# Performance work log

Measured on AMD Instinct MI355X. Metric: run time of the kernel, lower is better.

## Reference

```python
import jax, jax.numpy as jnp
import numpy as np

HEADS = 8
DIM_HEAD = 64
SCALE = DIM_HEAD ** (-0.5)


def setup_inputs() -> dict:
    key = jax.random.key(0)
    k1, k2, k3, k4 = jax.random.split(key, 4)
    B, H, W, n, dim = 2, 64, 64, 8, 512
    inner = HEADS * DIM_HEAD  # 512
    x = jax.random.normal(k1, (B, H, W, n, dim), dtype=jnp.float32)
    mask = jax.random.uniform(k2, (B, H, W, 1, n, n), dtype=jnp.float32)
    w_qkv = jax.random.normal(k3, (dim, 3 * inner), dtype=jnp.float32) * 0.02
    w_out = jax.random.normal(k4, (inner, dim), dtype=jnp.float32) * 0.02
    b_out = jnp.zeros((dim,), dtype=jnp.float32)
    return {"x": x, "mask": mask, "w_qkv": w_qkv, "w_out": w_out, "b_out": b_out}


def reference(x, mask, w_qkv, w_out, b_out):
    B, H, W, n, dim = x.shape
    inner = HEADS * DIM_HEAD
    qkv = x @ w_qkv  # [B,H,W,n,3*inner]
    q, k, v = jnp.split(qkv, 3, axis=-1)

    def to_heads(t):
        # 'B H W n (h d) -> B H W h n d'
        t = t.reshape(B, H, W, n, HEADS, DIM_HEAD)
        return jnp.swapaxes(t, 3, 4)

    q, k, v = to_heads(q), to_heads(k), to_heads(v)
    dots = jnp.einsum('bxyhnd,bxyhmd->bxyhnm', q, k) * SCALE
    dots = dots * mask  # multiplicative mask pre-softmax
    attn = jax.nn.softmax(dots, axis=-1)
    out = jnp.einsum('bxyhnm,bxyhmd->bxyhnd', attn, v)
    # 'B H W h n d -> B H W n (h d)'
    out = jnp.swapaxes(out, 3, 4).reshape(B, H, W, n, inner)
    return out @ w_out + b_out
```

## Files before the change

### kernel.cpp

```cpp
#include <hip/hip_runtime.h>
#include <hip/hip_bf16.h>

#define NROWS 65536
#define DIM   512
#define SCALE_ 0.125f

typedef short bf16x8 __attribute__((ext_vector_type(8)));
typedef unsigned short u16x8 __attribute__((ext_vector_type(8)));
typedef float f32x4 __attribute__((ext_vector_type(4)));

__device__ __forceinline__ unsigned short f2bf(float f) {
  union { float f; unsigned u; } v; v.f = f;
  unsigned r = v.u + 0x7FFFu + ((v.u >> 16) & 1u);
  return (unsigned short)(r >> 16);
}

#define GLL16(gptr, lptr) \
  __builtin_amdgcn_global_load_lds((const __attribute__((address_space(1))) void*)(gptr), \
                                   (__attribute__((address_space(3))) void*)(lptr), 16, 0, 0)

__global__ void prep_w_kernel(const float* __restrict__ wqkv,
                              const float* __restrict__ wout,
                              unsigned short* __restrict__ wqkvT,
                              unsigned short* __restrict__ woutT) {
  int idx = blockIdx.x * 256 + threadIdx.x;
  if (idx < 1536 * 512) {
    int j = idx >> 9, c = idx & 511;
    wqkvT[idx] = f2bf(wqkv[(size_t)c * 1536 + j]);
  } else {
    int k2 = idx - 1536 * 512;
    int n = k2 >> 9, c = k2 & 511;
    woutT[k2] = f2bf(wout[(size_t)c * 512 + n]);
  }
}

__global__ void prep_x_kernel(const float* __restrict__ x,
                              unsigned short* __restrict__ xb) {
  size_t i = ((size_t)blockIdx.x * 256 + threadIdx.x) * 8;
  float4 a = *(const float4*)(x + i);
  float4 b = *(const float4*)(x + i + 4);
  u16x8 p;
  p[0] = f2bf(a.x); p[1] = f2bf(a.y); p[2] = f2bf(a.z); p[3] = f2bf(a.w);
  p[4] = f2bf(b.x); p[5] = f2bf(b.y); p[6] = f2bf(b.z); p[7] = f2bf(b.w);
  *(u16x8*)(xb + i) = p;
}

template<int AMODE>
__global__ __launch_bounds__(256, 2)
void qkv_attn_kernel(const float* __restrict__ x,
                     const unsigned short* __restrict__ xb,
                     const float* __restrict__ mask,
                     const unsigned short* __restrict__ wqkvT,
                     unsigned short* __restrict__ attn_out) {
  __shared__ __align__(16) unsigned char smem[81920];

  const int t = threadIdx.x;
  const int lane = t & 63, wave = t >> 6;
  const int wm = wave >> 1, wn = wave & 1;
  const int fr = lane & 15, fq = lane >> 4;
  const int l8 = lane >> 3;
  const int cswz = ((lane & 7) ^ l8) * 8;

  const int per = gridDim.x >> 3;
  const int lin = (blockIdx.x & 7) * per + (blockIdx.x >> 3);
  const int mtile = lin >> 3, head = lin & 7;
  const int r0 = mtile * 128;

  f32x4 acc[4][6];
  const f32x4 z4 = {0.f, 0.f, 0.f, 0.f};
  #pragma unroll
  for (int m = 0; m < 4; ++m)
    #pragma unroll
    for (int n = 0; n < 6; ++n) acc[m][n] = z4;

  auto STAGE = [&](int buf, int kt2) {
    unsigned char* base = smem + buf * 40960;
    const int k0 = kt2 * 64;
    if constexpr (AMODE == 0) {
      const unsigned short* gA = xb + (size_t)(r0 + l8) * 512 + k0 + cswz;
      #pragma unroll
      for (int i = 0; i < 4; ++i) {
        int c = wave * 4 + i;
        GLL16(gA + (size_t)c * 8 * 512, base + c * 1024);
      }
    } else {
      #pragma unroll
      for (int i2 = 0; i2 < 8; ++i2) {
        int c = t + (i2 << 8);
        int row = c >> 4, q = c & 15;
        float4 v = *(const float4*)(x + (size_t)(r0 + row) * 512 + k0 + q * 4);
        ushort4 p;
        p.x = f2bf(v.x); p.y = f2bf(v.y); p.z = f2bf(v.z); p.w = f2bf(v.w);
        unsigned byte = (unsigned)row * 128 +
                        ((((unsigned)(q >> 1)) << 4) ^ (((unsigned)(row & 7)) << 4)) +
                        (unsigned)(q & 1) * 8;
        *(ushort4*)(base + byte) = p;
      }
    }
    const unsigned short* gB = wqkvT + k0 + cswz;
    #pragma unroll
    for (int i = 0; i < 6; ++i) {
      int c = wave * 6 + i;
      int n = c * 8 + l8;
      int jg = ((n >> 6) << 9) + head * 64 + (n & 63);
      GLL16(gB + (size_t)jg * 512, base + 16384 + c * 1024);
    }
  };

  STAGE(0, 0);
  asm volatile("s_waitcnt vmcnt(0)" ::: "memory");
  __syncthreads();
  int cur = 0;

  for (int kt = 0; kt < 8; ++kt) {
    if (kt < 7) STAGE(cur ^ 1, kt + 1);
    unsigned char* Ab = smem + cur * 40960;
    unsigned char* Bb = Ab + 16384;
    const unsigned xr = ((unsigned)(fr & 7)) << 4;
    #pragma unroll
    for (int kk = 0; kk < 2; ++kk) {
      const unsigned ko = ((unsigned)(kk * 64 + fq * 16)) ^ xr;
      bf16x8 a[4], b[6];
      #pragma unroll
      for (int m = 0; m < 4; ++m)
        a[m] = *(const bf16x8*)(Ab + (unsigned)(wm * 64 + m * 16 + fr) * 128 + ko);
      #pragma unroll
      for (int n = 0; n < 6; ++n)
        b[n] = *(const bf16x8*)(Bb + (unsigned)(wn * 96 + n * 16 + fr) * 128 + ko);
      #pragma unroll
      for (int m = 0; m < 4; ++m)
        #pragma unroll
        for (int n = 0; n < 6; ++n)
          acc[m][n] = __builtin_amdgcn_mfma_f32_16x16x32_bf16(a[m], b[n], acc[m][n], 0, 0, 0);
    }
    asm volatile("s_waitcnt vmcnt(0)" ::: "memory");
    __syncthreads();
    cur ^= 1;
  }

  unsigned short* Qs = (unsigned short*)smem;
  unsigned short* Ks = (unsigned short*)(smem + 16384);
  unsigned short* VT = (unsigned short*)(smem + 32768);
  unsigned short* Pl = (unsigned short*)(smem + 52224);

  {
    int d = t >> 2, q = t & 3;
    ushort4 z; z.x = 0; z.y = 0; z.z = 0; z.w = 0;
    *(ushort4*)(VT + d * 152 + 128 + q * 4) = z;
  }
  #pragma unroll
  for (int n = 0; n < 6; ++n) {
    int col = wn * 96 + n * 16 + fr;
    #pragma unroll
    for (int m = 0; m < 4; ++m) {
      if (col < 128) {
        unsigned short* T = (col < 64) ? Qs : Ks;
        unsigned cc = (unsigned)(col & 63);
        #pragma unroll
        for (int r = 0; r < 4; ++r) {
          int row = wm * 64 + m * 16 + fq * 4 + r;
          unsigned byte = (unsigned)row * 128 + ((cc * 2) ^ (((unsigned)(row & 7)) << 4));
          *(unsigned short*)((unsigned char*)T + byte) = f2bf(acc[m][n][r]);
        }
      } else {
        int d = col - 128;
        ushort4 p;
        p.x = f2bf(acc[m][n][0]); p.y = f2bf(acc[m][n][1]);
        p.z = f2bf(acc[m][n][2]); p.w = f2bf(acc[m][n][3]);
        *(ushort4*)(VT + d * 152 + (wm * 64 + m * 16 + fq * 4)) = p;
      }
    }
  }
  __syncthreads();

  #pragma unroll
  for (int pp = 0; pp < 2; ++pp) {
    const int pair = wave * 2 + pp;
    const unsigned rbyte = (unsigned)(pair * 16 + fr) * 128;
    const unsigned xrp = ((unsigned)(fr & 7)) << 4;
    f32x4 s = {0.f, 0.f, 0.f, 0.f};
    #pragma unroll
    for (int kk = 0; kk < 2; ++kk) {
      const unsigned ko = ((unsigned)(kk * 64 + fq * 16)) ^ xrp;
      bf16x8 qf = *(const bf16x8*)((unsigned char*)Qs + rbyte + ko);
      bf16x8 kf = *(const bf16x8*)((unsigned char*)Ks + rbyte + ko);
      s = __builtin_amdgcn_mfma_f32_16x16x32_bf16(qf, kf, s, 0, 0, 0);
    }
    float p4[4];
    #pragma unroll
    for (int r = 0; r < 4; ++r) {
      int row = fq * 4 + r;
      bool valid = (row >> 3) == (fr >> 3);
      int Pg = mtile * 16 + pair * 2 + (row >> 3);
      float mv = mask[(size_t)Pg * 64 + (row & 7) * 8 + (fr & 7)];
      p4[r] = valid ? s[r] * SCALE_ * mv : -3.0e38f;
    }
    #pragma unroll
    for (int r = 0; r < 4; ++r) {
      float v = p4[r];
      float mx = v;
      mx = fmaxf(mx, __shfl_xor(mx, 1));
      mx = fmaxf(mx, __shfl_xor(mx, 2));
      mx = fmaxf(mx, __shfl_xor(mx, 4));
      float e = __expf(v - mx);
      float sm = e;
      sm += __shfl_xor(sm, 1);
      sm += __shfl_xor(sm, 2);
      sm += __shfl_xor(sm, 4);
      p4[r] = e / sm;
    }
    #pragma unroll
    for (int r = 0; r < 4; ++r) {
      int row = fq * 4 + r;
      bool valid = (row >> 3) == (fr >> 3);
      Pl[pair * 640 + row * 40 + fr] = valid ? f2bf(p4[r]) : (unsigned short)0;
      Pl[pair * 640 + row * 40 + 16 + fr] = 0;
    }
    #pragma unroll
    for (int dblk = 0; dblk < 4; ++dblk) {
      bf16x8 af = *(const bf16x8*)((unsigned char*)VT +
                    (unsigned)(dblk * 16 + fr) * 304 + (unsigned)(pair * 32 + fq * 16));
      bf16x8 bf = *(const bf16x8*)((unsigned char*)Pl +
                    (unsigned)pair * 1280 + (unsigned)fr * 80 + (unsigned)fq * 16);
      f32x4 o = {0.f, 0.f, 0.f, 0.f};
      o = __builtin_amdgcn_mfma_f32_16x16x32_bf16(af, bf, o, 0, 0, 0);
      ushort4 pk;
      pk.x = f2bf(o[0]); pk.y = f2bf(o[1]); pk.z = f2bf(o[2]); pk.w = f2bf(o[3]);
      *(ushort4*)(attn_out + (size_t)(r0 + pair * 16 + fr) * 512 +
                  head * 64 + dblk * 16 + fq * 4) = pk;
    }
  }
}

__global__ __launch_bounds__(256, 2)
void outproj_kernel(const unsigned short* __restrict__ attn,
                    const unsigned short* __restrict__ woutT,
                    const float* __restrict__ bias,
                    float* __restrict__ out) {
  __shared__ __align__(16) unsigned short A2[128 * 72];
  __shared__ __align__(16) unsigned short B2[128 * 72];
  const int t = threadIdx.x;
  const int lane = t & 63, wave = t >> 6;
  const int wm = wave >> 1, wn = wave & 1;
  const int fr = lane & 15, fq = lane >> 4;

  const int per = gridDim.x >> 3;
  const int lin = (blockIdx.x & 7) * per + (blockIdx.x >> 3);
  const int mtile = lin >> 2, nt = lin & 3;
  const int r0 = mtile * 128, n0 = nt * 128;

  f32x4 acc[4][4];
  const f32x4 z4 = {0.f, 0.f, 0.f, 0.f};
  #pragma unroll
  for (int m = 0; m < 4; ++m)
    #pragma unroll
    for (int n = 0; n < 4; ++n) acc[m][n] = z4;

  for (int kt = 0; kt < 8; ++kt) {
    const int k0 = kt * 64;
    #pragma unroll
    for (int i2 = 0; i2 < 4; ++i2) {
      int c = t + (i2 << 8);
      int row = c >> 3, wi = c & 7;
      *(uint4*)(A2 + row * 72 + wi * 8) =
          *(const uint4*)(attn + (size_t)(r0 + row) * 512 + k0 + wi * 8);
      *(uint4*)(B2 + row * 72 + wi * 8) =
          *(const uint4*)(woutT + (size_t)(n0 + row) * 512 + k0 + wi * 8);
    }
    __syncthreads();
    #pragma unroll
    for (int kk = 0; kk < 2; ++kk) {
      const int krd = kk * 32 + fq * 8;
      bf16x8 a[4], b[4];
      #pragma unroll
      for (int m = 0; m < 4; ++m)
        a[m] = *(const bf16x8*)(A2 + (wm * 64 + m * 16 + fr) * 72 + krd);
      #pragma unroll
      for (int n = 0; n < 4; ++n)
        b[n] = *(const bf16x8*)(B2 + (wn * 64 + n * 16 + fr) * 72 + krd);
      #pragma unroll
      for (int m = 0; m < 4; ++m)
        #pragma unroll
        for (int n = 0; n < 4; ++n)
          acc[m][n] = __builtin_amdgcn_mfma_f32_16x16x32_bf16(a[m], b[n], acc[m][n], 0, 0, 0);
    }
    __syncthreads();
  }
  #pragma unroll
  for (int n = 0; n < 4; ++n) {
    int col = n0 + wn * 64 + n * 16 + fr;
    float bv = bias[col];
    #pragma unroll
    for (int m = 0; m < 4; ++m) {
      #pragma unroll
      for (int j = 0; j < 4; ++j) {
        int row = r0 + wm * 64 + m * 16 + fq * 4 + j;
        out[(size_t)row * 512 + col] = acc[m][n][j] + bv;
      }
    }
  }
}

extern "C" void kernel_launch(void* const* d_in, const int* in_sizes, int n_in,
                              void* d_out, int out_size, void* d_ws, size_t ws_size,
                              hipStream_t stream) {
  const float* x    = (const float*)d_in[0];
  const float* mask = (const float*)d_in[1];
  const float* wqkv = (const float*)d_in[2];
  const float* wout = (const float*)d_in[3];
  const float* bias = (const float*)d_in[4];
  float* out = (float*)d_out;

  unsigned char* ws = (unsigned char*)d_ws;
  unsigned short* attn  = (unsigned short*)ws;
  unsigned short* wqkvT = (unsigned short*)(ws + 67108864);
  unsigned short* woutT = (unsigned short*)(ws + 67108864 + 1572864);
  unsigned short* xb    = (unsigned short*)(ws + 67108864 + 1572864 + 524288);
  const size_t need_xb = 67108864ull + 1572864ull + 524288ull + 67108864ull;

  prep_w_kernel<<<4096, 256, 0, stream>>>(wqkv, wout, wqkvT, woutT);
  if (ws_size >= need_xb) {
    prep_x_kernel<<<16384, 256, 0, stream>>>(x, xb);
    qkv_attn_kernel<0><<<4096, 256, 0, stream>>>(x, xb, mask, wqkvT, attn);
  } else {
    qkv_attn_kernel<1><<<4096, 256, 0, stream>>>(x, xb, mask, wqkvT, attn);
  }
  outproj_kernel<<<2048, 256, 0, stream>>>(attn, woutT, bias, out);
}
```

Baseline: 238.9 us.

## Fuse x bf16 conversion into QKV kernel with register prefetch; double-buffer out-proj

Removes the separate fp32-to-bf16 pass over x. The QKV kernel now loads fp32 x tiles into registers one step ahead, converts them and writes them to LDS after the MFMA block, so the global loads overlap compute. The mask values are preloaded into registers at kernel start, and the output projection moves to double-buffered global_load_lds staging with a swizzled LDS layout. This saves a full read and write of the x tensor, at the cost of more registers in the QKV kernel and 8x more fp32 reads per tile than the bf16 path, since x is re-read by each of the 8 heads.

```diff
diff --git a/kernel.cpp b/kernel.cpp
--- a/kernel.cpp
+++ b/kernel.cpp
@@ -34,21 +34,8 @@
   }
 }
 
-__global__ void prep_x_kernel(const float* __restrict__ x,
-                              unsigned short* __restrict__ xb) {
-  size_t i = ((size_t)blockIdx.x * 256 + threadIdx.x) * 8;
-  float4 a = *(const float4*)(x + i);
-  float4 b = *(const float4*)(x + i + 4);
-  u16x8 p;
-  p[0] = f2bf(a.x); p[1] = f2bf(a.y); p[2] = f2bf(a.z); p[3] = f2bf(a.w);
-  p[4] = f2bf(b.x); p[5] = f2bf(b.y); p[6] = f2bf(b.z); p[7] = f2bf(b.w);
-  *(u16x8*)(xb + i) = p;
-}
-
-template<int AMODE>
 __global__ __launch_bounds__(256, 2)
 void qkv_attn_kernel(const float* __restrict__ x,
-                     const unsigned short* __restrict__ xb,
                      const float* __restrict__ mask,
                      const unsigned short* __restrict__ wqkvT,
                      unsigned short* __restrict__ attn_out) {
@@ -66,6 +53,18 @@
   const int mtile = lin >> 3, head = lin & 7;
   const int r0 = mtile * 128;
 
+  float mreg[2][4];
+  #pragma unroll
+  for (int pp = 0; pp < 2; ++pp) {
+    int pair = wave * 2 + pp;
+    #pragma unroll
+    for (int r = 0; r < 4; ++r) {
+      int row = fq * 4 + r;
+      int Pg = mtile * 16 + pair * 2 + (row >> 3);
+      mreg[pp][r] = mask[(size_t)Pg * 64 + (row & 7) * 8 + (fr & 7)];
+    }
+  }
+
   f32x4 acc[4][6];
   const f32x4 z4 = {0.f, 0.f, 0.f, 0.f};
   #pragma unroll
@@ -73,47 +72,50 @@
     #pragma unroll
     for (int n = 0; n < 6; ++n) acc[m][n] = z4;
 
-  auto STAGE = [&](int buf, int kt2) {
+  float4 va[8];
+  const int arow = t >> 4, aq = t & 15;
+  const unsigned abyte = (unsigned)arow * 128 +
+                         ((((unsigned)(aq >> 1)) << 4) ^ (((unsigned)(arow & 7)) << 4)) +
+                         (unsigned)(aq & 1) * 8;
+
+  auto LOAD_A = [&](int kt2) {
+    const int k0 = kt2 * 64;
+    const float* gx = x + (size_t)(r0 + arow) * 512 + k0 + aq * 4;
+    #pragma unroll
+    for (int i2 = 0; i2 < 8; ++i2)
+      va[i2] = *(const float4*)(gx + (size_t)i2 * 16 * 512);
+  };
+  auto WRITE_A = [&](int buf) {
     unsigned char* base = smem + buf * 40960;
-    const int k0 = kt2 * 64;
-    if constexpr (AMODE == 0) {
-      const unsigned short* gA = xb + (size_t)(r0 + l8) * 512 + k0 + cswz;
-      #pragma unroll
-      for (int i = 0; i < 4; ++i) {
-        int c = wave * 4 + i;
-        GLL16(gA + (size_t)c * 8 * 512, base + c * 1024);
-      }
-    } else {
-      #pragma unroll
-      for (int i2 = 0; i2 < 8; ++i2) {
-        int c = t + (i2 << 8);
-        int row = c >> 4, q = c & 15;
-        float4 v = *(const float4*)(x + (size_t)(r0 + row) * 512 + k0 + q * 4);
-        ushort4 p;
-        p.x = f2bf(v.x); p.y = f2bf(v.y); p.z = f2bf(v.z); p.w = f2bf(v.w);
-        unsigned byte = (unsigned)row * 128 +
-                        ((((unsigned)(q >> 1)) << 4) ^ (((unsigned)(row & 7)) << 4)) +
-                        (unsigned)(q & 1) * 8;
-        *(ushort4*)(base + byte) = p;
-      }
-    }
-    const unsigned short* gB = wqkvT + k0 + cswz;
+    #pragma unroll
+    for (int i2 = 0; i2 < 8; ++i2) {
+      ushort4 p;
+      p.x = f2bf(va[i2].x); p.y = f2bf(va[i2].y);
+      p.z = f2bf(va[i2].z); p.w = f2bf(va[i2].w);
+      *(ushort4*)(base + abyte + (unsigned)i2 * 2048) = p;
+    }
+  };
+  auto STAGE_B = [&](int buf, int kt2) {
+    unsigned char* base = smem + buf * 40960 + 16384;
+    const unsigned short* gB = wqkvT + kt2 * 64 + cswz;
     #pragma unroll
     for (int i = 0; i < 6; ++i) {
       int c = wave * 6 + i;
       int n = c * 8 + l8;
       int jg = ((n >> 6) << 9) + head * 64 + (n & 63);
-      GLL16(gB + (size_t)jg * 512, base + 16384 + c * 1024);
+      GLL16(gB + (size_t)jg * 512, base + c * 1024);
     }
   };
 
-  STAGE(0, 0);
+  LOAD_A(0);
+  STAGE_B(0, 0);
+  WRITE_A(0);
   asm volatile("s_waitcnt vmcnt(0)" ::: "memory");
   __syncthreads();
   int cur = 0;
 
   for (int kt = 0; kt < 8; ++kt) {
-    if (kt < 7) STAGE(cur ^ 1, kt + 1);
+    if (kt < 7) { LOAD_A(kt + 1); STAGE_B(cur ^ 1, kt + 1); }
     unsigned char* Ab = smem + cur * 40960;
     unsigned char* Bb = Ab + 16384;
     const unsigned xr = ((unsigned)(fr & 7)) << 4;
@@ -133,6 +135,7 @@
         for (int n = 0; n < 6; ++n)
           acc[m][n] = __builtin_amdgcn_mfma_f32_16x16x32_bf16(a[m], b[n], acc[m][n], 0, 0, 0);
     }
+    if (kt < 7) WRITE_A(cur ^ 1);
     asm volatile("s_waitcnt vmcnt(0)" ::: "memory");
     __syncthreads();
     cur ^= 1;
@@ -191,9 +194,7 @@
     for (int r = 0; r < 4; ++r) {
       int row = fq * 4 + r;
       bool valid = (row >> 3) == (fr >> 3);
-      int Pg = mtile * 16 + pair * 2 + (row >> 3);
-      float mv = mask[(size_t)Pg * 64 + (row & 7) * 8 + (fr & 7)];
-      p4[r] = valid ? s[r] * SCALE_ * mv : -3.0e38f;
+      p4[r] = valid ? s[r] * SCALE_ * mreg[pp][r] : -3.0e38f;
     }
     #pragma unroll
     for (int r = 0; r < 4; ++r) {
@@ -237,12 +238,13 @@
                     const unsigned short* __restrict__ woutT,
                     const float* __restrict__ bias,
                     float* __restrict__ out) {
-  __shared__ __align__(16) unsigned short A2[128 * 72];
-  __shared__ __align__(16) unsigned short B2[128 * 72];
+  __shared__ __align__(16) unsigned char smem[65536];
   const int t = threadIdx.x;
   const int lane = t & 63, wave = t >> 6;
   const int wm = wave >> 1, wn = wave & 1;
   const int fr = lane & 15, fq = lane >> 4;
+  const int l8 = lane >> 3;
+  const int cswz = ((lane & 7) ^ l8) * 8;
 
   const int per = gridDim.x >> 3;
   const int lin = (blockIdx.x & 7) * per + (blockIdx.x >> 3);
@@ -256,35 +258,48 @@
     #pragma unroll
     for (int n = 0; n < 4; ++n) acc[m][n] = z4;
 
+  auto STAGE = [&](int buf, int kt2) {
+    unsigned char* base = smem + buf * 32768;
+    const int k0 = kt2 * 64;
+    const unsigned short* gA = attn  + (size_t)(r0 + l8) * 512 + k0 + cswz;
+    const unsigned short* gB = woutT + (size_t)(n0 + l8) * 512 + k0 + cswz;
+    #pragma unroll
+    for (int i = 0; i < 4; ++i) {
+      int c = wave * 4 + i;
+      GLL16(gA + (size_t)c * 8 * 512, base + c * 1024);
+      GLL16(gB + (size_t)c * 8 * 512, base + 16384 + c * 1024);
+    }
+  };
+
+  STAGE(0, 0);
+  asm volatile("s_waitcnt vmcnt(0)" ::: "memory");
+  __syncthreads();
+  int cur = 0;
+
   for (int kt = 0; kt < 8; ++kt) {
-    const int k0 = kt * 64;
-    #pragma unroll
-    for (int i2 = 0; i2 < 4; ++i2) {
-      int c = t + (i2 << 8);
-      int row = c >> 3, wi = c & 7;
-      *(uint4*)(A2 + row * 72 + wi * 8) =
-          *(const uint4*)(attn + (size_t)(r0 + row) * 512 + k0 + wi * 8);
-      *(uint4*)(B2 + row * 72 + wi * 8) =
-          *(const uint4*)(woutT + (size_t)(n0 + row) * 512 + k0 + wi * 8);
-    }
-    __syncthreads();
+    if (kt < 7) STAGE(cur ^ 1, kt + 1);
+    unsigned char* Ab = smem + cur * 32768;
+    unsigned char* Bb = Ab + 16384;
+    const unsigned xr = ((unsigned)(fr & 7)) << 4;
     #pragma unroll
     for (int kk = 0; kk < 2; ++kk) {
-      const int krd = kk * 32 + fq * 8;
+      const unsigned ko = ((unsigned)(kk * 64 + fq * 16)) ^ xr;
       bf16x8 a[4], b[4];
       #pragma unroll
       for (int m = 0; m < 4; ++m)
-        a[m] = *(const bf16x8*)(A2 + (wm * 64 + m * 16 + fr) * 72 + krd);
+        a[m] = *(const bf16x8*)(Ab + (unsigned)(wm * 64 + m * 16 + fr) * 128 + ko);
       #pragma unroll
       for (int n = 0; n < 4; ++n)
-        b[n] = *(const bf16x8*)(B2 + (wn * 64 + n * 16 + fr) * 72 + krd);
+        b[n] = *(const bf16x8*)(Bb + (unsigned)(wn * 64 + n * 16 + fr) * 128 + ko);
       #pragma unroll
       for (int m = 0; m < 4; ++m)
         #pragma unroll
         for (int n = 0; n < 4; ++n)
           acc[m][n] = __builtin_amdgcn_mfma_f32_16x16x32_bf16(a[m], b[n], acc[m][n], 0, 0, 0);
     }
+    asm volatile("s_waitcnt vmcnt(0)" ::: "memory");
     __syncthreads();
+    cur ^= 1;
   }
   #pragma unroll
   for (int n = 0; n < 4; ++n) {
@@ -315,15 +330,8 @@
   unsigned short* attn  = (unsigned short*)ws;
   unsigned short* wqkvT = (unsigned short*)(ws + 67108864);
   unsigned short* woutT = (unsigned short*)(ws + 67108864 + 1572864);
-  unsigned short* xb    = (unsigned short*)(ws + 67108864 + 1572864 + 524288);
-  const size_t need_xb = 67108864ull + 1572864ull + 524288ull + 67108864ull;
 
   prep_w_kernel<<<4096, 256, 0, stream>>>(wqkv, wout, wqkvT, woutT);
-  if (ws_size >= need_xb) {
-    prep_x_kernel<<<16384, 256, 0, stream>>>(x, xb);
-    qkv_attn_kernel<0><<<4096, 256, 0, stream>>>(x, xb, mask, wqkvT, attn);
-  } else {
-    qkv_attn_kernel<1><<<4096, 256, 0, stream>>>(x, xb, mask, wqkvT, attn);
-  }
+  qkv_attn_kernel<<<4096, 256, 0, stream>>>(x, mask, wqkvT, attn);
   outproj_kernel<<<2048, 256, 0, stream>>>(attn, woutT, bias, out);
 }
```

Measured after the change: 278.5 us. +16.6%, slower.
